# Kernel tuning notes

Hardware: AMD Instinct MI355X
Metric: run time of the kernel (lower is better)

Reference implementation:

```python
import jax, jax.numpy as jnp
import numpy as np

B, P, ENC = 32, 197, 768
EMB, HID, ATT = 512, 512, 256
VOCAB, SLEN = 32000, 41


def setup_inputs() -> dict:
    key = jax.random.key(0)
    ks = jax.random.split(key, 24)
    s = lambda *sh: 1.0 / np.sqrt(sh[0])
    inp = {
        'encoder_out': jax.random.normal(ks[0], (B, P, ENC), dtype=jnp.float32),
        'captions': jax.random.randint(ks[1], (B, SLEN), 0, VOCAB),
        'emb': jax.random.normal(ks[2], (VOCAB, EMB), dtype=jnp.float32) * 0.02,
        # attention
        'W_ea': jax.random.normal(ks[3], (ENC, ATT), dtype=jnp.float32) * s(ENC),
        'b_ea': jnp.zeros((ATT,), jnp.float32),
        'W_da': jax.random.normal(ks[4], (HID, ATT), dtype=jnp.float32) * s(HID),
        'b_da': jnp.zeros((ATT,), jnp.float32),
        'w_fa': jax.random.normal(ks[5], (ATT,), dtype=jnp.float32) * s(ATT),
        'b_fa': jnp.zeros((), jnp.float32),
        # init h/c from mean encoder
        'W_inh': jax.random.normal(ks[6], (ENC, HID), dtype=jnp.float32) * s(ENC),
        'b_inh': jnp.zeros((HID,), jnp.float32),
        'W_inc': jax.random.normal(ks[7], (ENC, HID), dtype=jnp.float32) * s(ENC),
        'b_inc': jnp.zeros((HID,), jnp.float32),
        # gate
        'W_fb': jax.random.normal(ks[8], (HID, ENC), dtype=jnp.float32) * s(HID),
        'b_fb': jnp.zeros((ENC,), jnp.float32),
        # LSTMCell (PyTorch gate order: i, f, g, o)
        'W_ih': jax.random.normal(ks[9], (EMB + ENC, 4 * HID), dtype=jnp.float32) * s(EMB + ENC),
        'b_ih': jnp.zeros((4 * HID,), jnp.float32),
        'W_hh': jax.random.normal(ks[10], (HID, 4 * HID), dtype=jnp.float32) * s(HID),
        'b_hh': jnp.zeros((4 * HID,), jnp.float32),
        # output projection
        'W_out': jax.random.normal(ks[11], (HID, VOCAB), dtype=jnp.float32) * s(HID),
        'b_out': jnp.zeros((VOCAB,), jnp.float32),
    }
    return inp


def reference(encoder_out, captions, emb, W_ea, b_ea, W_da, b_da, w_fa, b_fa,
              W_inh, b_inh, W_inc, b_inc, W_fb, b_fb,
              W_ih, b_ih, W_hh, b_hh, W_out, b_out):
    # dropout is identity (eval mode / p used only in training stochasticity)
    mean_enc = encoder_out.mean(axis=1)                     # (B, ENC)
    h0 = mean_enc @ W_inh + b_inh                           # (B, HID)
    c0 = mean_enc @ W_inc + b_inc
    att1 = encoder_out @ W_ea + b_ea                        # (B, P, ATT) step-invariant
    embs = emb[captions]                                    # (B, S, EMB)
    T = captions.shape[1] - 1
    xs = jnp.swapaxes(embs[:, :T, :], 0, 1)                 # (T, B, EMB)

    def step(carry, x_t):
        h, c = carry
        att2 = h @ W_da + b_da                              # (B, ATT)
        e = jax.nn.relu(att1 + att2[:, None, :]) @ w_fa + b_fa  # (B, P)
        alpha = jax.nn.softmax(e, axis=1)
        awe = jnp.einsum('bp,bpd->bd', alpha, encoder_out)  # (B, ENC)
        gate = jax.nn.sigmoid(h @ W_fb + b_fb)
        awe = gate * awe
        lstm_in = jnp.concatenate([x_t, awe], axis=1)       # (B, EMB+ENC)
        gates = lstm_in @ W_ih + b_ih + h @ W_hh + b_hh     # (B, 4*HID)
        i, f, g, o = jnp.split(gates, 4, axis=1)
        c_new = jax.nn.sigmoid(f) * c + jax.nn.sigmoid(i) * jnp.tanh(g)
        h_new = jax.nn.sigmoid(o) * jnp.tanh(c_new)
        preds = h_new @ W_out + b_out                       # (B, VOCAB)
        return (h_new, c_new), preds

    _, preds = jax.lax.scan(step, (h0, c0), xs)             # (T, B, VOCAB)
    return jnp.swapaxes(preds, 0, 1)                        # (B, T, VOCAB)
```

## Files before the change

kernel.cpp:

```cpp
#include <hip/hip_runtime.h>

#define Bz   32
#define Pz   197
#define ENCz 768
#define EMBz 512
#define HIDz 512
#define ATTz 256
#define VOCz 32000
#define Tz   40

#define NBLK 224

typedef unsigned short ushort_t;
typedef __attribute__((ext_vector_type(8))) short frag_ab;
typedef __attribute__((ext_vector_type(4))) float frag_cd;
typedef __attribute__((ext_vector_type(4))) ushort_t ushort4v;
typedef __attribute__((ext_vector_type(8))) ushort_t ushort8v;

#define MFMA16(a, b, c) __builtin_amdgcn_mfma_f32_16x16x32_bf16((a), (b), (c), 0, 0, 0)

__device__ __forceinline__ float b2f(ushort_t u) {
    return __uint_as_float(((unsigned)u) << 16);
}
__device__ __forceinline__ ushort_t f2bf(float f) {
    unsigned u = __float_as_uint(f);
    unsigned r = (u + 0x7fffu + ((u >> 16) & 1u)) >> 16;
    return (ushort_t)r;
}
__device__ __forceinline__ float sigf(float x) { return 1.f / (1.f + __expf(-x)); }
__device__ __forceinline__ float tanhfast(float x) { return 1.f - 2.f / (__expf(2.f * x) + 1.f); }

__device__ __forceinline__ void st_f32(float* p, float v) {
    __hip_atomic_store(p, v, __ATOMIC_RELAXED, __HIP_MEMORY_SCOPE_AGENT);
}
__device__ __forceinline__ float ld_f32(const float* p) {
    return __hip_atomic_load(p, __ATOMIC_RELAXED, __HIP_MEMORY_SCOPE_AGENT);
}
__device__ __forceinline__ void st_u32(unsigned* p, unsigned v) {
    __hip_atomic_store(p, v, __ATOMIC_RELAXED, __HIP_MEMORY_SCOPE_AGENT);
}
__device__ __forceinline__ unsigned ld_u32(const unsigned* p) {
    return __hip_atomic_load(p, __ATOMIC_RELAXED, __HIP_MEMORY_SCOPE_AGENT);
}
__device__ __forceinline__ frag_ab ldfrag(const ushort_t* p) {
    union { frag_ab f; unsigned long long q[2]; } u;
    u.q[0] = __hip_atomic_load((const unsigned long long*)p, __ATOMIC_RELAXED, __HIP_MEMORY_SCOPE_AGENT);
    u.q[1] = __hip_atomic_load((const unsigned long long*)(p + 4), __ATOMIC_RELAXED, __HIP_MEMORY_SCOPE_AGENT);
    return u.f;
}
__device__ __forceinline__ void arrive(unsigned* slot, unsigned v, int tid) {
    __syncthreads();
    if (tid == 0) {
        asm volatile("s_waitcnt vmcnt(0)" ::: "memory");
        st_u32(slot, v);
    }
}

__global__ void k_binit(unsigned* f) {
    for (int i = threadIdx.x; i < 11264; i += 256) f[i] = 0u;
}

__global__ __launch_bounds__(256) void k_prep(const float* __restrict__ enc, ushort_t* __restrict__ encB,
                                              float* __restrict__ meanE, ushort_t* __restrict__ encTb) {
    __shared__ float tile[32][33];
    const int bid = blockIdx.x, tid = threadIdx.x;
    if (bid < 2364) {
        size_t base = ((size_t)bid * 256 + tid) * 8;
        const float4* src = (const float4*)(enc + base);
        float4 a = src[0], b = src[1];
        ushort8v v;
        v[0] = f2bf(a.x); v[1] = f2bf(a.y); v[2] = f2bf(a.z); v[3] = f2bf(a.w);
        v[4] = f2bf(b.x); v[5] = f2bf(b.y); v[6] = f2bf(b.z); v[7] = f2bf(b.w);
        *(ushort8v*)(encB + base) = v;
    } else if (bid < 2460) {
        int e = (bid - 2364) * 256 + tid;
        int b = e / ENCz, d = e % ENCz;
        const float* p = enc + (size_t)b * Pz * ENCz + d;
        float s = 0.f;
        for (int i = 0; i < Pz; ++i) s += p[i * ENCz];
        meanE[e] = s * (1.f / (float)Pz);
    } else {
        int idx = bid - 2460;
        int d0 = (idx % 24) * 32; int rest = idx / 24;
        int p0 = (rest % 7) * 32; int b = rest / 7;
        int tx = tid & 31, ty = tid >> 5;
#pragma unroll
        for (int i = 0; i < 4; ++i) {
            int p = p0 + ty + i * 8;
            tile[ty + i * 8][tx] = (p < Pz) ? enc[((size_t)b * Pz + p) * ENCz + d0 + tx] : 0.f;
        }
        __syncthreads();
#pragma unroll
        for (int i = 0; i < 4; ++i) {
            int d = d0 + ty + i * 8, p = p0 + tx;
            if (p < 200) encTb[((size_t)b * ENCz + d) * 200 + p] = f2bf(tile[tx][ty + i * 8]);
        }
    }
}

__global__ __launch_bounds__(256) void k_h0c0(const float* __restrict__ meanE,
                                              const float* __restrict__ W_inh, const float* __restrict__ b_inh,
                                              const float* __restrict__ W_inc, const float* __restrict__ b_inc,
                                              float* __restrict__ c_cur, ushort_t* __restrict__ Abuf) {
    __shared__ float msh[ENCz];
    int bid = blockIdx.x, tid = threadIdx.x;
    int b = bid >> 2, seg = bid & 3;
    for (int i = tid; i < ENCz; i += 256) msh[i] = meanE[b * ENCz + i];
    __syncthreads();
    int col = (seg & 1) * 256 + tid;
    bool isc = (seg >> 1) != 0;
    const float* W = isc ? W_inc : W_inh;
    const float* bb = isc ? b_inc : b_inh;
    float a0 = 0.f, a1 = 0.f, a2 = 0.f, a3 = 0.f;
    for (int k = 0; k < ENCz; k += 4) {
        a0 += msh[k + 0] * W[(k + 0) * HIDz + col];
        a1 += msh[k + 1] * W[(k + 1) * HIDz + col];
        a2 += msh[k + 2] * W[(k + 2) * HIDz + col];
        a3 += msh[k + 3] * W[(k + 3) * HIDz + col];
    }
    float acc = a0 + a1 + a2 + a3 + bb[col];
    if (isc) c_cur[b * HIDz + col] = acc;
    else Abuf[b * 1280 + 768 + col] = f2bf(acc);
}

__global__ __launch_bounds__(128) void k_gather(const int* __restrict__ captions, const float* __restrict__ emb,
                                                ushort_t* __restrict__ Xemb) {
    int row = blockIdx.x;
    int t = row >> 5, b = row & 31;
    int cap = captions[b * 41 + t];
    float4 f = *(const float4*)(emb + (size_t)cap * EMBz + threadIdx.x * 4);
    ushort4v v; v[0] = f2bf(f.x); v[1] = f2bf(f.y); v[2] = f2bf(f.z); v[3] = f2bf(f.w);
    *(ushort4v*)(Xemb + (size_t)row * EMBz + threadIdx.x * 4) = v;
}

__global__ __launch_bounds__(256) void k_transpose(const float* __restrict__ in, int R, int C,
                                                   ushort_t* __restrict__ out, int ldo, int koff) {
    __shared__ ushort_t tile[32][33];
    int c0 = blockIdx.x * 32, r0 = blockIdx.y * 32;
    int tx = threadIdx.x & 31, ty = threadIdx.x >> 5;
#pragma unroll
    for (int i = 0; i < 4; ++i) {
        int r = r0 + ty + i * 8;
        tile[ty + i * 8][tx] = f2bf(in[(size_t)r * C + c0 + tx]);
    }
    __syncthreads();
#pragma unroll
    for (int i = 0; i < 4; ++i) {
        int c = c0 + ty + i * 8;
        out[(size_t)c * ldo + koff + r0 + tx] = tile[tx][ty + i * 8];
    }
}

template <int MODE>
__global__ __launch_bounds__(256) void k_gemm(const ushort_t* __restrict__ A, int lda, int M,
                                              const ushort_t* __restrict__ BT, int K,
                                              const float* __restrict__ B1, const float* __restrict__ B2,
                                              void* __restrict__ out, int ldo) {
    __shared__ __align__(16) ushort_t As[128 * 64];
    __shared__ __align__(16) ushort_t Bs[128 * 64];
    const int tid = threadIdx.x;
    const int lane = tid & 63, w = tid >> 6;
    const int wm = w >> 1, wn = w & 1;
    int n0, m0;
    if (MODE == 2) {
        const int total = gridDim.x * gridDim.y;
        const int lin = blockIdx.y * gridDim.x + blockIdx.x;
        const int q = total >> 3, r = total - (q << 3);
        const int xcd = lin & 7, slot = lin >> 3;
        const int L = (xcd < r) ? xcd * (q + 1) + slot : r * (q + 1) + (xcd - r) * q + slot;
        const int nIdx = L / (int)gridDim.y;
        n0 = nIdx * 128; m0 = (L - nIdx * (int)gridDim.y) * 128;
    } else {
        n0 = blockIdx.x * 128; m0 = blockIdx.y * 128;
    }
    const int quad = lane >> 4, c16 = lane & 15;

    frag_cd acc[4][4];
#pragma unroll
    for (int i = 0; i < 4; ++i)
#pragma unroll
        for (int j = 0; j < 4; ++j) acc[i][j] = (frag_cd){0.f, 0.f, 0.f, 0.f};

    for (int k0 = 0; k0 < K; k0 += 64) {
#pragma unroll
        for (int it = 0; it < 4; ++it) {
            int c = tid + it * 256;
            int row = c >> 3, col8 = (c & 7) * 8;
            int gr = m0 + row; gr = gr < M ? gr : M - 1;
            *(frag_ab*)&As[row * 64 + col8] = *(const frag_ab*)&A[(size_t)gr * lda + k0 + col8];
            *(frag_ab*)&Bs[row * 64 + col8] = *(const frag_ab*)&BT[(size_t)(n0 + row) * K + k0 + col8];
        }
        __syncthreads();
#pragma unroll
        for (int kk = 0; kk < 64; kk += 32) {
            int kcol = kk + quad * 8;
            frag_ab af[4], bf[4];
#pragma unroll
            for (int i = 0; i < 4; ++i) af[i] = *(const frag_ab*)&As[(wm * 64 + i * 16 + c16) * 64 + kcol];
#pragma unroll
            for (int j = 0; j < 4; ++j) bf[j] = *(const frag_ab*)&Bs[(wn * 64 + j * 16 + c16) * 64 + kcol];
#pragma unroll
            for (int i = 0; i < 4; ++i)
#pragma unroll
                for (int j = 0; j < 4; ++j) acc[i][j] = MFMA16(af[i], bf[j], acc[i][j]);
        }
        __syncthreads();
    }

#pragma unroll
    for (int i = 0; i < 4; ++i) {
#pragma unroll
        for (int j = 0; j < 4; ++j) {
            int n = n0 + wn * 64 + j * 16 + c16;
            float bias = B1[n];
            if (B2 != nullptr) bias += B2[n];
#pragma unroll
            for (int r = 0; r < 4; ++r) {
                int m = m0 + wm * 64 + i * 16 + quad * 4 + r;
                float v = acc[i][j][r] + bias;
                if (MODE == 0) {
                    if (m < M) ((float*)out)[(size_t)m * ldo + n] = v;
                } else if (MODE == 1) {
                    if (m < M) ((ushort_t*)out)[(size_t)m * ldo + n] = f2bf(v);
                } else {
                    int b = m & 31, t = m >> 5;
                    ((float*)out)[(size_t)b * (Tz * VOCz) + (size_t)t * VOCz + n] = v;
                }
            }
        }
    }
}

__device__ __forceinline__ void gate_calc(const ushort_t* __restrict__ W_preT, const float* __restrict__ b_fb,
                                          const float* hsh, int d0, float* gate_out, int tid) {
    if (tid < 192) {
        const int d = tid >> 1, half = tid & 1;
        const ushort_t* wr = W_preT + (size_t)(256 + d0 + d) * 512 + half * 256;
        const float* hh = hsh + half * 256;
        float a0 = 0.f, a1 = 0.f;
        for (int k = 0; k < 256; k += 8) {
            ushort8v wv8 = *(const ushort8v*)&wr[k];
#pragma unroll
            for (int x = 0; x < 8; ++x) {
                float f = b2f(wv8[x]) * hh[k + x];
                if (x & 1) a1 += f; else a0 += f;
            }
        }
        float s = a0 + a1;
        s += __shfl_xor(s, 1, 64);
        if (half == 0) gate_out[d] = sigf(s + b_fb[d0 + d]);
    }
}

__device__ __forceinline__ void awe_dot(const ushort_t* encS, const float* gate_l, const float* alpha_l,
                                        ushort_t* dst, int tid) {
    if (tid < 192) {
        const int d = tid >> 1, h = tid & 1;
        const int c0 = h ? 13 : 0, c1 = h ? 25 : 13;
        float s = 0.f;
        for (int c = c0; c < c1; ++c) {
            ushort8v v = *(const ushort8v*)&encS[d * 200 + c * 8];
#pragma unroll
            for (int jj = 0; jj < 8; ++jj) s += b2f(v[jj]) * alpha_l[c * 8 + jj];
        }
        s += __shfl_xor(s, 1, 64);
        float gs = s * gate_l[d];
        unsigned pk = f2bf(gs);
        unsigned nb = __shfl_down(pk, 2, 64);
        if ((tid & 3) == 0) st_u32((unsigned*)(dst + d), pk | (nb << 16));
    }
}

__global__ __launch_bounds__(256, 1) void k_recur(
    const ushort_t* __restrict__ att1, const ushort_t* __restrict__ encTb,
    const ushort_t* __restrict__ W_preT, const float* __restrict__ b_da,
    const float* __restrict__ b_fb, const float* __restrict__ w_fa,
    const float* __restrict__ b_fa, const ushort_t* __restrict__ WgT,
    const float* __restrict__ Xih, const float* __restrict__ c0,
    ushort_t* __restrict__ Abuf, float* __restrict__ alpha_buf,
    ushort_t* __restrict__ Hall, unsigned* __restrict__ barflags)
{
    __shared__ __align__(16) char smem[126208];
    float* scratch = (float*)smem;
    char* R = smem + 8192;

    unsigned* flagS = barflags;
    unsigned* flagA = barflags + 4096;
    unsigned* flagE = barflags + 10240;

    const int g = (int)blockIdx.x;
    const int tid = (int)threadIdx.x;
    const int lane = tid & 63, wv = tid >> 6;
    const int quad = lane >> 4, c16 = lane & 15;

    const bool isS3 = (g < 128);
    const bool isE  = (g >= 192);
    const bool dual = (g >= 128 && g < 192);
    const int j0 = g << 2;
    const int task0 = g;
    const int task1 = dual ? 192 + (g - 128) : 0;
    const int b0 = task0 >> 3, d0 = (task0 & 7) * 96;
    const int b1 = task1 >> 3, d1 = (task1 & 7) * 96;
    const int eb = g - 192;

    ushort_t (*Wl)[1288] = (ushort_t(*)[1288])R;
    ushort_t* enc0  = isS3 ? (ushort_t*)(R + 41216) : (ushort_t*)R;
    ushort_t* enc1  = (ushort_t*)(R + 38400);
    ushort_t* att1L = (ushort_t*)R;

    if (isS3) {
        int r = tid >> 4, ch = tid & 15;
        int coln = ((r >> 2) << 9) + j0 + (r & 3);
        const ushort_t* src = WgT + (size_t)coln * 1280 + ch * 80;
        ushort_t* dst = &Wl[r][ch * 80];
#pragma unroll
        for (int i = 0; i < 10; ++i)
            *(ushort8v*)(dst + i * 8) = *(const ushort8v*)(src + i * 8);
    }
    if (!isE) {
        const ushort_t* src = encTb + ((size_t)(b0 * 768 + (task0 & 7) * 96)) * 200;
        for (int i = 0; i < 10; ++i) {
            int c = tid + i * 256;
            if (c < 2400) *(ushort8v*)&enc0[c * 8] = *(const ushort8v*)&src[c * 8];
        }
        if (dual) {
            const ushort_t* src1 = encTb + ((size_t)(b1 * 768 + (task1 & 7) * 96)) * 200;
            for (int i = 0; i < 10; ++i) {
                int c = tid + i * 256;
                if (c < 2400) *(ushort8v*)&enc1[c * 8] = *(const ushort8v*)&src1[c * 8];
            }
        }
    } else {
        for (int i = 0; i < 25; ++i) {
            int c = tid + i * 256;
            if (c < 6304) {
                int p = c >> 5, off = (c & 31) * 8;
                *(ushort8v*)&att1L[p * 264 + off] = *(const ushort8v*)&att1[((size_t)(eb * Pz + p)) * 256 + off];
            }
        }
    }
    float creg = 0.f;
    if (isS3 && tid < 128) creg = c0[(tid >> 2) * HIDz + j0 + (tid & 3)];
    __syncthreads();

    for (int t = 0; t < Tz; ++t) {
        ushort_t* Ab_r = Abuf + (size_t)(t & 1) * 40960;
        ushort_t* Ab_w = Abuf + (size_t)((t + 1) & 1) * 40960;
        const unsigned epoch = (unsigned)(t + 1);

        if (isE) {
            if (t) {
                if (tid < 128) while (ld_u32(&flagS[tid << 5]) < (unsigned)t) __builtin_amdgcn_s_sleep(1);
                __syncthreads();
            }
            if (tid < 64) {
                frag_ab v = ldfrag(Ab_r + eb * 1280 + 768 + tid * 8);
#pragma unroll
                for (int i = 0; i < 8; ++i) scratch[tid * 8 + i] = b2f((ushort_t)v[i]);
            }
            __syncthreads();
            {
                const ushort_t* wr = W_preT + (size_t)tid * 512;
                float a0 = 0.f, a1 = 0.f, a2 = 0.f, a3 = 0.f;
                for (int k = 0; k < 512; k += 16) {
                    ushort8v w0 = *(const ushort8v*)&wr[k];
                    ushort8v w1 = *(const ushort8v*)&wr[k + 8];
#pragma unroll
                    for (int x = 0; x < 8; ++x) {
                        float f0 = b2f(w0[x]) * scratch[k + x];
                        float f1 = b2f(w1[x]) * scratch[k + 8 + x];
                        if (x & 1) { a1 += f0; a3 += f1; } else { a0 += f0; a2 += f1; }
                    }
                }
                scratch[512 + tid] = (a0 + a1) + (a2 + a3) + b_da[tid];
                scratch[768 + tid] = w_fa[tid];
            }
            __syncthreads();
            float ev = -3.0e38f;
            if (tid < Pz) {
                const ushort_t* ar = att1L + tid * 264;
                float s = 0.f;
#pragma unroll
                for (int j8 = 0; j8 < 256; j8 += 8) {
                    ushort8v v = *(const ushort8v*)&ar[j8];
#pragma unroll
                    for (int jj = 0; jj < 8; ++jj)
                        s += fmaxf(b2f(v[jj]) + scratch[512 + j8 + jj], 0.f) * scratch[768 + j8 + jj];
                }
                ev = s + b_fa[0];
            }
            float mv = ev;
            for (int o = 32; o; o >>= 1) mv = fmaxf(mv, __shfl_down(mv, o, 64));
            if (lane == 0) scratch[1024 + wv] = mv;
            __syncthreads();
            const float mx = fmaxf(fmaxf(scratch[1024], scratch[1025]), fmaxf(scratch[1026], scratch[1027]));
            float ex = (tid < Pz) ? __expf(ev - mx) : 0.f;
            float sv = ex;
            for (int o = 32; o; o >>= 1) sv += __shfl_down(sv, o, 64);
            if (lane == 0) scratch[1028 + wv] = sv;
            __syncthreads();
            const float inv = 1.f / (scratch[1028] + scratch[1029] + scratch[1030] + scratch[1031]);
            if (tid < 200) st_f32(&alpha_buf[eb * 200 + tid], ex * inv);
            arrive(&flagE[eb << 5], epoch, tid);
        } else {
            if (t) {
                if (tid < 128) while (ld_u32(&flagS[tid << 5]) < (unsigned)t) __builtin_amdgcn_s_sleep(1);
                __syncthreads();
            }
            if (tid < 64) {
                frag_ab v = ldfrag(Ab_r + b0 * 1280 + 768 + tid * 8);
#pragma unroll
                for (int i = 0; i < 8; ++i) scratch[tid * 8 + i] = b2f((ushort_t)v[i]);
            }
            if (dual && tid >= 64 && tid < 128) {
                int tt = tid - 64;
                frag_ab v = ldfrag(Ab_r + b1 * 1280 + 768 + tt * 8);
#pragma unroll
                for (int i = 0; i < 8; ++i) scratch[512 + tt * 8 + i] = b2f((ushort_t)v[i]);
            }
            __syncthreads();
            gate_calc(W_preT, b_fb, scratch, d0, scratch + 1024, tid);
            if (dual) gate_calc(W_preT, b_fb, scratch + 512, d1, scratch + 1120, tid);
            __syncthreads();
            if (tid == 0)  while (ld_u32(&flagE[b0 << 5]) < epoch) __builtin_amdgcn_s_sleep(1);
            if (dual && tid == 32) while (ld_u32(&flagE[b1 << 5]) < epoch) __builtin_amdgcn_s_sleep(1);
            __syncthreads();
            if (tid < 200) scratch[1280 + tid] = ld_f32(&alpha_buf[b0 * 200 + tid]);
            __syncthreads();
            awe_dot(enc0, scratch + 1024, scratch + 1280, Ab_r + b0 * 1280 + d0, tid);
            if (dual) {
                __syncthreads();
                if (tid < 200) scratch[1280 + tid] = ld_f32(&alpha_buf[b1 * 200 + tid]);
                __syncthreads();
                awe_dot(enc1, scratch + 1120, scratch + 1280, Ab_r + b1 * 1280 + d1, tid);
            }
            arrive(&flagA[g << 5], epoch, tid);
        }

        if (isS3) {
            if (tid < 192) while (ld_u32(&flagA[tid << 5]) < epoch) __builtin_amdgcn_s_sleep(1);
            __syncthreads();
            frag_cd p0 = (frag_cd){0.f, 0.f, 0.f, 0.f};
            frag_cd p1 = (frag_cd){0.f, 0.f, 0.f, 0.f};
            const ushort_t* Ar0 = Ab_r + (size_t)c16 * 1280 + wv * 320 + quad * 8;
            const ushort_t* Ar1 = Ar0 + 16 * 1280;
            const ushort_t* Wr = &Wl[c16][wv * 320 + quad * 8];
#pragma unroll
            for (int ks = 0; ks < 10; ++ks) {
                frag_ab bfr = *(const frag_ab*)(Wr + ks * 32);
                p0 = MFMA16(ldfrag(Ar0 + ks * 32), bfr, p0);
                p1 = MFMA16(ldfrag(Ar1 + ks * 32), bfr, p1);
            }
#pragma unroll
            for (int r = 0; r < 4; ++r) {
                scratch[wv * 512 + (quad * 4 + r) * 16 + c16] = p0[r];
                scratch[wv * 512 + 256 + (quad * 4 + r) * 16 + c16] = p1[r];
            }
            __syncthreads();
            float s0, s1;
            {
                const int mr = tid >> 4, col = tid & 15;
                const int base = mr * 16 + col;
                const int xcol = ((col >> 2) << 9) + j0 + (col & 3);
                s0 = scratch[base] + scratch[512 + base] + scratch[1024 + base] + scratch[1536 + base]
                   + Xih[(size_t)t * 65536 + mr * 2048 + xcol];
                s1 = scratch[256 + base] + scratch[768 + base] + scratch[1280 + base] + scratch[1792 + base]
                   + Xih[(size_t)t * 65536 + (16 + mr) * 2048 + xcol];
            }
            __syncthreads();
            scratch[tid] = s0;
            scratch[256 + tid] = s1;
            __syncthreads();
            if (tid < 128) {
                const int bl = tid >> 2, jj = tid & 3, j = j0 + jj;
                const float iv = scratch[bl * 16 + jj], fv = scratch[bl * 16 + 4 + jj];
                const float gv = scratch[bl * 16 + 8 + jj], ov = scratch[bl * 16 + 12 + jj];
                const float cn = sigf(fv) * creg + sigf(iv) * tanhfast(gv);
                creg = cn;
                const float hn = sigf(ov) * tanhfast(cn);
                const ushort_t hb = f2bf(hn);
                Hall[((size_t)t * 32 + bl) * HIDz + j] = hb;
                unsigned pk = hb;
                unsigned nb = __shfl_down(pk, 1, 64);
                if ((tid & 1) == 0)
                    st_u32((unsigned*)(Ab_w + bl * 1280 + 768 + j), pk | (nb << 16));
            }
            arrive(&flagS[g << 5], epoch, tid);
        }
    }
}

extern "C" void kernel_launch(void* const* d_in, const int* in_sizes, int n_in,
                              void* d_out, int out_size, void* d_ws, size_t ws_size,
                              hipStream_t stream) {
    const float* enc   = (const float*)d_in[0];
    const int*   caps  = (const int*)d_in[1];
    const float* emb   = (const float*)d_in[2];
    const float* W_ea  = (const float*)d_in[3];
    const float* b_ea  = (const float*)d_in[4];
    const float* W_da  = (const float*)d_in[5];
    const float* b_da  = (const float*)d_in[6];
    const float* w_fa  = (const float*)d_in[7];
    const float* b_fa  = (const float*)d_in[8];
    const float* W_inh = (const float*)d_in[9];
    const float* b_inh = (const float*)d_in[10];
    const float* W_inc = (const float*)d_in[11];
    const float* b_inc = (const float*)d_in[12];
    const float* W_fb  = (const float*)d_in[13];
    const float* b_fb  = (const float*)d_in[14];
    const float* W_ih  = (const float*)d_in[15];
    const float* b_ih  = (const float*)d_in[16];
    const float* W_hh  = (const float*)d_in[17];
    const float* b_hh  = (const float*)d_in[18];
    const float* W_out = (const float*)d_in[19];
    const float* b_out = (const float*)d_in[20];

    char* ws = (char*)d_ws;
    ushort_t* att1     = (ushort_t*)(ws + 0);
    ushort_t* Xemb     = (ushort_t*)(ws + 3227648);
    ushort_t* encB     = (ushort_t*)(ws + 4538368);
    float*    Xih      = (float*)(ws + 14221312);
    float*    meanE    = (float*)(ws + 24707072);
    float*    c_cur    = (float*)(ws + 24805376);
    ushort_t* Abuf     = (ushort_t*)(ws + 24870912);
    float*    alpha_buf= (float*)(ws + 25165824);
    ushort_t* Hall     = (ushort_t*)(ws + 25191424);
    ushort_t* WgT      = (ushort_t*)(ws + 26502144);
    ushort_t* W_preT   = (ushort_t*)(ws + 31745024);
    ushort_t* W_eaT    = (ushort_t*)(ws + 32793600);
    ushort_t* W_ihxT   = (ushort_t*)(ws + 33186816);
    ushort_t* W_outT   = (ushort_t*)(ws + 35283968);
    ushort_t* encTb    = (ushort_t*)(ws + 68051968);
    unsigned* barflags = (unsigned*)(ws + 77882368);

    k_binit<<<1, 256, 0, stream>>>(barflags);
    k_prep<<<7836, 256, 0, stream>>>(enc, encB, meanE, encTb);
    k_h0c0<<<128, 256, 0, stream>>>(meanE, W_inh, b_inh, W_inc, b_inc, c_cur, Abuf);
    k_gather<<<1280, 128, 0, stream>>>(caps, emb, Xemb);
    k_transpose<<<dim3(8, 24), 256, 0, stream>>>(W_ea, 768, 256, W_eaT, 768, 0);
    k_transpose<<<dim3(64, 16), 256, 0, stream>>>(W_ih, 512, 2048, W_ihxT, 512, 0);
    k_transpose<<<dim3(64, 24), 256, 0, stream>>>(W_ih + 512 * 2048, 768, 2048, WgT, 1280, 0);
    k_transpose<<<dim3(64, 16), 256, 0, stream>>>(W_hh, 512, 2048, WgT, 1280, 768);
    k_transpose<<<dim3(8, 16), 256, 0, stream>>>(W_da, 512, 256, W_preT, 512, 0);
    k_transpose<<<dim3(24, 16), 256, 0, stream>>>(W_fb, 512, 768, W_preT + 256 * 512, 512, 0);
    k_transpose<<<dim3(1000, 16), 256, 0, stream>>>(W_out, 512, 32000, W_outT, 512, 0);

    k_gemm<1><<<dim3(2, 50), 256, 0, stream>>>(encB, 768, 6304, W_eaT, 768, b_ea, nullptr, att1, 256);
    k_gemm<0><<<dim3(16, 10), 256, 0, stream>>>(Xemb, 512, 1280, W_ihxT, 512, b_ih, b_hh, Xih, 2048);

    hipLaunchKernelGGL(k_recur, dim3(NBLK), dim3(256), 0, stream,
                       att1, encTb, W_preT, b_da, b_fb, w_fa, b_fa, WgT, Xih,
                       c_cur, Abuf, alpha_buf, Hall, barflags);

    k_gemm<2><<<dim3(250, 10), 256, 0, stream>>>(Hall, 512, 1280, W_outT, 512, b_out, nullptr, d_out, VOCz);
}
```

Baseline: 1.462 ms.

## Restructure recurrent kernel into 32 uniform 1024-thread blocks with phased global barriers

The persistent recurrence kernel goes from 224 specialised 256-thread blocks (attention, awe and LSTM roles with separate flag sets) to 32 identical 1024-thread blocks, one per batch row. Each timestep now runs three grid-wide barrier phases. The first is an MFMA pre-projection of h into att2 and the gate. The second does softmax attention plus the gated awe for one batch row, reading encTb directly from global instead of staging it in LDS. The third is an MFMA LSTM gate GEMM over 16 hidden columns per block. The goal is a simpler barrier structure with fewer waiting blocks and more work per block. The cost is three full barriers per step and much lower CU occupancy, since only 32 of the available CUs are used.

```diff
diff --git a/kernel.cpp b/kernel.cpp
--- a/kernel.cpp
+++ b/kernel.cpp
@@ -9,8 +9,6 @@
 #define VOCz 32000
 #define Tz   40
 
-#define NBLK 224
-
 typedef unsigned short ushort_t;
 typedef __attribute__((ext_vector_type(8))) short frag_ab;
 typedef __attribute__((ext_vector_type(4))) float frag_cd;
@@ -57,7 +55,7 @@
 }
 
 __global__ void k_binit(unsigned* f) {
-    for (int i = threadIdx.x; i < 11264; i += 256) f[i] = 0u;
+    for (int i = threadIdx.x; i < 1024; i += 256) f[i] = 0u;
 }
 
 __global__ __launch_bounds__(256) void k_prep(const float* __restrict__ enc, ushort_t* __restrict__ encB,
@@ -101,7 +99,7 @@
 __global__ __launch_bounds__(256) void k_h0c0(const float* __restrict__ meanE,
                                               const float* __restrict__ W_inh, const float* __restrict__ b_inh,
                                               const float* __restrict__ W_inc, const float* __restrict__ b_inc,
-                                              float* __restrict__ c_cur, ushort_t* __restrict__ Abuf) {
+                                              float* __restrict__ c_cur, ushort_t* __restrict__ hbuf) {
     __shared__ float msh[ENCz];
     int bid = blockIdx.x, tid = threadIdx.x;
     int b = bid >> 2, seg = bid & 3;
@@ -120,7 +118,7 @@
     }
     float acc = a0 + a1 + a2 + a3 + bb[col];
     if (isc) c_cur[b * HIDz + col] = acc;
-    else Abuf[b * 1280 + 768 + col] = f2bf(acc);
+    else hbuf[b * HIDz + col] = f2bf(acc);
 }
 
 __global__ __launch_bounds__(128) void k_gather(const int* __restrict__ captions, const float* __restrict__ emb,
@@ -231,262 +229,159 @@
     }
 }
 
-__device__ __forceinline__ void gate_calc(const ushort_t* __restrict__ W_preT, const float* __restrict__ b_fb,
-                                          const float* hsh, int d0, float* gate_out, int tid) {
-    if (tid < 192) {
-        const int d = tid >> 1, half = tid & 1;
-        const ushort_t* wr = W_preT + (size_t)(256 + d0 + d) * 512 + half * 256;
-        const float* hh = hsh + half * 256;
-        float a0 = 0.f, a1 = 0.f;
-        for (int k = 0; k < 256; k += 8) {
-            ushort8v wv8 = *(const ushort8v*)&wr[k];
-#pragma unroll
-            for (int x = 0; x < 8; ++x) {
-                float f = b2f(wv8[x]) * hh[k + x];
-                if (x & 1) a1 += f; else a0 += f;
-            }
-        }
-        float s = a0 + a1;
-        s += __shfl_xor(s, 1, 64);
-        if (half == 0) gate_out[d] = sigf(s + b_fb[d0 + d]);
-    }
-}
-
-__device__ __forceinline__ void awe_dot(const ushort_t* encS, const float* gate_l, const float* alpha_l,
-                                        ushort_t* dst, int tid) {
-    if (tid < 192) {
-        const int d = tid >> 1, h = tid & 1;
-        const int c0 = h ? 13 : 0, c1 = h ? 25 : 13;
-        float s = 0.f;
-        for (int c = c0; c < c1; ++c) {
-            ushort8v v = *(const ushort8v*)&encS[d * 200 + c * 8];
-#pragma unroll
-            for (int jj = 0; jj < 8; ++jj) s += b2f(v[jj]) * alpha_l[c * 8 + jj];
-        }
-        s += __shfl_xor(s, 1, 64);
-        float gs = s * gate_l[d];
-        unsigned pk = f2bf(gs);
-        unsigned nb = __shfl_down(pk, 2, 64);
-        if ((tid & 3) == 0) st_u32((unsigned*)(dst + d), pk | (nb << 16));
-    }
-}
-
-__global__ __launch_bounds__(256, 1) void k_recur(
+__global__ __launch_bounds__(1024, 1) void k_recur(
     const ushort_t* __restrict__ att1, const ushort_t* __restrict__ encTb,
     const ushort_t* __restrict__ W_preT, const float* __restrict__ b_da,
     const float* __restrict__ b_fb, const float* __restrict__ w_fa,
     const float* __restrict__ b_fa, const ushort_t* __restrict__ WgT,
     const float* __restrict__ Xih, const float* __restrict__ c0,
-    ushort_t* __restrict__ Abuf, float* __restrict__ alpha_buf,
-    ushort_t* __restrict__ Hall, unsigned* __restrict__ barflags)
+    float* __restrict__ pre_buf, ushort_t* __restrict__ gawe_buf,
+    ushort_t* __restrict__ hbuf, ushort_t* __restrict__ Hall,
+    unsigned* __restrict__ flags)
 {
-    __shared__ __align__(16) char smem[126208];
-    float* scratch = (float*)smem;
-    char* R = smem + 8192;
-
-    unsigned* flagS = barflags;
-    unsigned* flagA = barflags + 4096;
-    unsigned* flagE = barflags + 10240;
+    __shared__ __align__(16) ushort_t att1L[197 * 264];
+    __shared__ float wfa_sh[256];
+    __shared__ float att2_sh[256];
+    __shared__ float gate_sh[768];
+    __shared__ float alpha_sh[200];
+    __shared__ float g4[2][4][32][16];
+    __shared__ float red[16];
 
     const int g = (int)blockIdx.x;
     const int tid = (int)threadIdx.x;
     const int lane = tid & 63, wv = tid >> 6;
     const int quad = lane >> 4, c16 = lane & 15;
 
-    const bool isS3 = (g < 128);
-    const bool isE  = (g >= 192);
-    const bool dual = (g >= 128 && g < 192);
-    const int j0 = g << 2;
-    const int task0 = g;
-    const int task1 = dual ? 192 + (g - 128) : 0;
-    const int b0 = task0 >> 3, d0 = (task0 & 7) * 96;
-    const int b1 = task1 >> 3, d1 = (task1 & 7) * 96;
-    const int eb = g - 192;
-
-    ushort_t (*Wl)[1288] = (ushort_t(*)[1288])R;
-    ushort_t* enc0  = isS3 ? (ushort_t*)(R + 41216) : (ushort_t*)R;
-    ushort_t* enc1  = (ushort_t*)(R + 38400);
-    ushort_t* att1L = (ushort_t*)R;
-
-    if (isS3) {
-        int r = tid >> 4, ch = tid & 15;
-        int coln = ((r >> 2) << 9) + j0 + (r & 3);
-        const ushort_t* src = WgT + (size_t)coln * 1280 + ch * 80;
-        ushort_t* dst = &Wl[r][ch * 80];
-#pragma unroll
-        for (int i = 0; i < 10; ++i)
-            *(ushort8v*)(dst + i * 8) = *(const ushort8v*)(src + i * 8);
-    }
-    if (!isE) {
-        const ushort_t* src = encTb + ((size_t)(b0 * 768 + (task0 & 7) * 96)) * 200;
-        for (int i = 0; i < 10; ++i) {
-            int c = tid + i * 256;
-            if (c < 2400) *(ushort8v*)&enc0[c * 8] = *(const ushort8v*)&src[c * 8];
-        }
-        if (dual) {
-            const ushort_t* src1 = encTb + ((size_t)(b1 * 768 + (task1 & 7) * 96)) * 200;
-            for (int i = 0; i < 10; ++i) {
-                int c = tid + i * 256;
-                if (c < 2400) *(ushort8v*)&enc1[c * 8] = *(const ushort8v*)&src1[c * 8];
-            }
-        }
-    } else {
-        for (int i = 0; i < 25; ++i) {
-            int c = tid + i * 256;
-            if (c < 6304) {
-                int p = c >> 5, off = (c & 31) * 8;
-                *(ushort8v*)&att1L[p * 264 + off] = *(const ushort8v*)&att1[((size_t)(eb * Pz + p)) * 256 + off];
-            }
-        }
-    }
+    for (int i = 0; i < 7; ++i) {
+        int c = tid + i * 1024;
+        if (c < 6304) {
+            int p = c >> 5, off = (c & 31) * 8;
+            *(ushort8v*)&att1L[p * 264 + off] =
+                *(const ushort8v*)&att1[((size_t)(g * Pz + p)) * 256 + off];
+        }
+    }
+    if (tid < 256) wfa_sh[tid] = w_fa[tid];
     float creg = 0.f;
-    if (isS3 && tid < 128) creg = c0[(tid >> 2) * HIDz + j0 + (tid & 3)];
+    if (tid < 512) creg = c0[(tid >> 4) * HIDz + g * 16 + (tid & 15)];
+    const float bfa = b_fa[0];
     __syncthreads();
 
     for (int t = 0; t < Tz; ++t) {
-        ushort_t* Ab_r = Abuf + (size_t)(t & 1) * 40960;
-        ushort_t* Ab_w = Abuf + (size_t)((t + 1) & 1) * 40960;
-        const unsigned epoch = (unsigned)(t + 1);
-
-        if (isE) {
-            if (t) {
-                if (tid < 128) while (ld_u32(&flagS[tid << 5]) < (unsigned)t) __builtin_amdgcn_s_sleep(1);
-                __syncthreads();
-            }
-            if (tid < 64) {
-                frag_ab v = ldfrag(Ab_r + eb * 1280 + 768 + tid * 8);
-#pragma unroll
-                for (int i = 0; i < 8; ++i) scratch[tid * 8 + i] = b2f((ushort_t)v[i]);
-            }
+        if (t) {
+            if (tid < 32) while (ld_u32(&flags[tid << 5]) < (unsigned)(3 * t)) __builtin_amdgcn_s_sleep(2);
             __syncthreads();
-            {
-                const ushort_t* wr = W_preT + (size_t)tid * 512;
-                float a0 = 0.f, a1 = 0.f, a2 = 0.f, a3 = 0.f;
-                for (int k = 0; k < 512; k += 16) {
-                    ushort8v w0 = *(const ushort8v*)&wr[k];
-                    ushort8v w1 = *(const ushort8v*)&wr[k + 8];
-#pragma unroll
-                    for (int x = 0; x < 8; ++x) {
-                        float f0 = b2f(w0[x]) * scratch[k + x];
-                        float f1 = b2f(w1[x]) * scratch[k + 8 + x];
-                        if (x & 1) { a1 += f0; a3 += f1; } else { a0 += f0; a2 += f1; }
-                    }
-                }
-                scratch[512 + tid] = (a0 + a1) + (a2 + a3) + b_da[tid];
-                scratch[768 + tid] = w_fa[tid];
-            }
-            __syncthreads();
-            float ev = -3.0e38f;
-            if (tid < Pz) {
-                const ushort_t* ar = att1L + tid * 264;
-                float s = 0.f;
-#pragma unroll
-                for (int j8 = 0; j8 < 256; j8 += 8) {
-                    ushort8v v = *(const ushort8v*)&ar[j8];
-#pragma unroll
-                    for (int jj = 0; jj < 8; ++jj)
-                        s += fmaxf(b2f(v[jj]) + scratch[512 + j8 + jj], 0.f) * scratch[768 + j8 + jj];
-                }
-                ev = s + b_fa[0];
-            }
-            float mv = ev;
-            for (int o = 32; o; o >>= 1) mv = fmaxf(mv, __shfl_down(mv, o, 64));
-            if (lane == 0) scratch[1024 + wv] = mv;
-            __syncthreads();
-            const float mx = fmaxf(fmaxf(scratch[1024], scratch[1025]), fmaxf(scratch[1026], scratch[1027]));
-            float ex = (tid < Pz) ? __expf(ev - mx) : 0.f;
-            float sv = ex;
-            for (int o = 32; o; o >>= 1) sv += __shfl_down(sv, o, 64);
-            if (lane == 0) scratch[1028 + wv] = sv;
-            __syncthreads();
-            const float inv = 1.f / (scratch[1028] + scratch[1029] + scratch[1030] + scratch[1031]);
-            if (tid < 200) st_f32(&alpha_buf[eb * 200 + tid], ex * inv);
-            arrive(&flagE[eb << 5], epoch, tid);
-        } else {
-            if (t) {
-                if (tid < 128) while (ld_u32(&flagS[tid << 5]) < (unsigned)t) __builtin_amdgcn_s_sleep(1);
-                __syncthreads();
-            }
-            if (tid < 64) {
-                frag_ab v = ldfrag(Ab_r + b0 * 1280 + 768 + tid * 8);
-#pragma unroll
-                for (int i = 0; i < 8; ++i) scratch[tid * 8 + i] = b2f((ushort_t)v[i]);
-            }
-            if (dual && tid >= 64 && tid < 128) {
-                int tt = tid - 64;
-                frag_ab v = ldfrag(Ab_r + b1 * 1280 + 768 + tt * 8);
-#pragma unroll
-                for (int i = 0; i < 8; ++i) scratch[512 + tt * 8 + i] = b2f((ushort_t)v[i]);
-            }
-            __syncthreads();
-            gate_calc(W_preT, b_fb, scratch, d0, scratch + 1024, tid);
-            if (dual) gate_calc(W_preT, b_fb, scratch + 512, d1, scratch + 1120, tid);
-            __syncthreads();
-            if (tid == 0)  while (ld_u32(&flagE[b0 << 5]) < epoch) __builtin_amdgcn_s_sleep(1);
-            if (dual && tid == 32) while (ld_u32(&flagE[b1 << 5]) < epoch) __builtin_amdgcn_s_sleep(1);
-            __syncthreads();
-            if (tid < 200) scratch[1280 + tid] = ld_f32(&alpha_buf[b0 * 200 + tid]);
-            __syncthreads();
-            awe_dot(enc0, scratch + 1024, scratch + 1280, Ab_r + b0 * 1280 + d0, tid);
-            if (dual) {
-                __syncthreads();
-                if (tid < 200) scratch[1280 + tid] = ld_f32(&alpha_buf[b1 * 200 + tid]);
-                __syncthreads();
-                awe_dot(enc1, scratch + 1120, scratch + 1280, Ab_r + b1 * 1280 + d1, tid);
-            }
-            arrive(&flagA[g << 5], epoch, tid);
-        }
-
-        if (isS3) {
-            if (tid < 192) while (ld_u32(&flagA[tid << 5]) < epoch) __builtin_amdgcn_s_sleep(1);
-            __syncthreads();
-            frag_cd p0 = (frag_cd){0.f, 0.f, 0.f, 0.f};
-            frag_cd p1 = (frag_cd){0.f, 0.f, 0.f, 0.f};
-            const ushort_t* Ar0 = Ab_r + (size_t)c16 * 1280 + wv * 320 + quad * 8;
-            const ushort_t* Ar1 = Ar0 + 16 * 1280;
-            const ushort_t* Wr = &Wl[c16][wv * 320 + quad * 8];
-#pragma unroll
-            for (int ks = 0; ks < 10; ++ks) {
-                frag_ab bfr = *(const frag_ab*)(Wr + ks * 32);
-                p0 = MFMA16(ldfrag(Ar0 + ks * 32), bfr, p0);
-                p1 = MFMA16(ldfrag(Ar1 + ks * 32), bfr, p1);
-            }
+        }
+        if (wv < 4) {
+            const int mt = wv >> 1, nt = wv & 1;
+            frag_cd acc = (frag_cd){0.f, 0.f, 0.f, 0.f};
+            const ushort_t* hrow = hbuf + (size_t)(mt * 16 + c16) * HIDz;
+            const ushort_t* wrow = W_preT + (size_t)(g * 32 + nt * 16 + c16) * HIDz;
+#pragma unroll
+            for (int kk = 0; kk < 512; kk += 32) {
+                frag_ab af = ldfrag(hrow + kk + quad * 8);
+                frag_ab bf = *(const frag_ab*)&wrow[kk + quad * 8];
+                acc = MFMA16(af, bf, acc);
+            }
+            const int n = g * 32 + nt * 16 + c16;
+            const float bias = (n < 256) ? b_da[n] : b_fb[n - 256];
 #pragma unroll
             for (int r = 0; r < 4; ++r) {
-                scratch[wv * 512 + (quad * 4 + r) * 16 + c16] = p0[r];
-                scratch[wv * 512 + 256 + (quad * 4 + r) * 16 + c16] = p1[r];
-            }
-            __syncthreads();
-            float s0, s1;
-            {
-                const int mr = tid >> 4, col = tid & 15;
-                const int base = mr * 16 + col;
-                const int xcol = ((col >> 2) << 9) + j0 + (col & 3);
-                s0 = scratch[base] + scratch[512 + base] + scratch[1024 + base] + scratch[1536 + base]
-                   + Xih[(size_t)t * 65536 + mr * 2048 + xcol];
-                s1 = scratch[256 + base] + scratch[768 + base] + scratch[1280 + base] + scratch[1792 + base]
-                   + Xih[(size_t)t * 65536 + (16 + mr) * 2048 + xcol];
-            }
-            __syncthreads();
-            scratch[tid] = s0;
-            scratch[256 + tid] = s1;
-            __syncthreads();
-            if (tid < 128) {
-                const int bl = tid >> 2, jj = tid & 3, j = j0 + jj;
-                const float iv = scratch[bl * 16 + jj], fv = scratch[bl * 16 + 4 + jj];
-                const float gv = scratch[bl * 16 + 8 + jj], ov = scratch[bl * 16 + 12 + jj];
-                const float cn = sigf(fv) * creg + sigf(iv) * tanhfast(gv);
-                creg = cn;
-                const float hn = sigf(ov) * tanhfast(cn);
-                const ushort_t hb = f2bf(hn);
-                Hall[((size_t)t * 32 + bl) * HIDz + j] = hb;
-                unsigned pk = hb;
-                unsigned nb = __shfl_down(pk, 1, 64);
-                if ((tid & 1) == 0)
-                    st_u32((unsigned*)(Ab_w + bl * 1280 + 768 + j), pk | (nb << 16));
-            }
-            arrive(&flagS[g << 5], epoch, tid);
-        }
+                int m = mt * 16 + quad * 4 + r;
+                float v = acc[r] + bias;
+                if (n >= 256) v = sigf(v);
+                st_f32(&pre_buf[m * 1024 + n], v);
+            }
+        }
+        arrive(&flags[g << 5], (unsigned)(3 * t + 1), tid);
+
+        if (tid < 32) while (ld_u32(&flags[tid << 5]) < (unsigned)(3 * t + 1)) __builtin_amdgcn_s_sleep(2);
+        __syncthreads();
+        if (tid < 256) att2_sh[tid] = ld_f32(&pre_buf[g * 1024 + tid]);
+        else gate_sh[tid - 256] = ld_f32(&pre_buf[g * 1024 + tid]);
+        __syncthreads();
+        float ev = -3.0e38f;
+        if (tid < Pz) {
+            const ushort_t* ar = att1L + tid * 264;
+            float s = 0.f;
+#pragma unroll
+            for (int j8 = 0; j8 < 256; j8 += 8) {
+                ushort8v v = *(const ushort8v*)&ar[j8];
+#pragma unroll
+                for (int jj = 0; jj < 8; ++jj)
+                    s += fmaxf(b2f(v[jj]) + att2_sh[j8 + jj], 0.f) * wfa_sh[j8 + jj];
+            }
+            ev = s + bfa;
+        }
+        float mv = ev;
+        for (int o = 32; o; o >>= 1) mv = fmaxf(mv, __shfl_down(mv, o, 64));
+        if (lane == 0 && wv < 4) red[wv] = mv;
+        __syncthreads();
+        const float mx = fmaxf(fmaxf(red[0], red[1]), fmaxf(red[2], red[3]));
+        float ex = (tid < Pz) ? __expf(ev - mx) : 0.f;
+        float sv = ex;
+        for (int o = 32; o; o >>= 1) sv += __shfl_down(sv, o, 64);
+        if (lane == 0 && wv < 4) red[4 + wv] = sv;
+        __syncthreads();
+        const float inv = 1.f / (red[4] + red[5] + red[6] + red[7]);
+        if (tid < 200) alpha_sh[tid] = (tid < Pz) ? ex * inv : 0.f;
+        __syncthreads();
+        if (tid < 768) {
+            const ushort_t* er = encTb + ((size_t)(g * ENCz + tid)) * 200;
+            float s = 0.f;
+#pragma unroll
+            for (int c = 0; c < 25; ++c) {
+                ushort8v v = *(const ushort8v*)&er[c * 8];
+#pragma unroll
+                for (int jj = 0; jj < 8; ++jj) s += b2f(v[jj]) * alpha_sh[c * 8 + jj];
+            }
+            float gs = s * gate_sh[tid];
+            unsigned pk = f2bf(gs);
+            unsigned nb = __shfl_down(pk, 1, 64);
+            if ((tid & 1) == 0) st_u32((unsigned*)&gawe_buf[g * 768 + tid], pk | (nb << 16));
+        }
+        arrive(&flags[g << 5], (unsigned)(3 * t + 2), tid);
+
+        if (tid < 32) while (ld_u32(&flags[tid << 5]) < (unsigned)(3 * t + 2)) __builtin_amdgcn_s_sleep(2);
+        __syncthreads();
+        {
+            const int kh = wv & 1, q = (wv >> 1) & 3, mt = wv >> 3;
+            frag_cd acc = (frag_cd){0.f, 0.f, 0.f, 0.f};
+            const int jcol = q * 512 + g * 16 + c16;
+            const ushort_t* wrow = WgT + (size_t)jcol * 1280;
+            const int arow = mt * 16 + c16;
+            const ushort_t* grow = gawe_buf + (size_t)arow * 768;
+            const ushort_t* hrow = hbuf + (size_t)arow * 512;
+#pragma unroll
+            for (int ki = 0; ki < 20; ++ki) {
+                const int k = kh * 640 + ki * 32;
+                frag_ab af = (k < 768) ? ldfrag(grow + k + quad * 8)
+                                       : ldfrag(hrow + (k - 768) + quad * 8);
+                frag_ab bf = *(const frag_ab*)&wrow[k + quad * 8];
+                acc = MFMA16(af, bf, acc);
+            }
+#pragma unroll
+            for (int r = 0; r < 4; ++r)
+                g4[kh][q][mt * 16 + quad * 4 + r][c16] = acc[r];
+        }
+        __syncthreads();
+        if (tid < 512) {
+            const int m = tid >> 4, jj = tid & 15;
+            const float* xr = Xih + (size_t)t * 65536 + m * 2048 + g * 16 + jj;
+            const float iv = g4[0][0][m][jj] + g4[1][0][m][jj] + xr[0];
+            const float fv = g4[0][1][m][jj] + g4[1][1][m][jj] + xr[512];
+            const float gv = g4[0][2][m][jj] + g4[1][2][m][jj] + xr[1024];
+            const float ov = g4[0][3][m][jj] + g4[1][3][m][jj] + xr[1536];
+            const float cn = sigf(fv) * creg + sigf(iv) * tanhfast(gv);
+            creg = cn;
+            const float hn = sigf(ov) * tanhfast(cn);
+            const ushort_t hb = f2bf(hn);
+            Hall[((size_t)t * 32 + m) * HIDz + g * 16 + jj] = hb;
+            unsigned pk = hb;
+            unsigned nb = __shfl_down(pk, 1, 64);
+            if ((tid & 1) == 0)
+                st_u32((unsigned*)&hbuf[m * 512 + g * 16 + jj], pk | (nb << 16));
+        }
+        arrive(&flags[g << 5], (unsigned)(3 * t + 3), tid);
     }
 }
 
@@ -522,8 +417,10 @@
     float*    Xih      = (float*)(ws + 14221312);
     float*    meanE    = (float*)(ws + 24707072);
     float*    c_cur    = (float*)(ws + 24805376);
-    ushort_t* Abuf     = (ushort_t*)(ws + 24870912);
-    float*    alpha_buf= (float*)(ws + 25165824);
+    float*    pre_buf  = (float*)(ws + 24870912);
+    ushort_t* gawe_buf = (ushort_t*)(ws + 25001984);
+    ushort_t* hbuf     = (ushort_t*)(ws + 25051136);
+    unsigned* flags    = (unsigned*)(ws + 25083904);
     ushort_t* Hall     = (ushort_t*)(ws + 25191424);
     ushort_t* WgT      = (ushort_t*)(ws + 26502144);
     ushort_t* W_preT   = (ushort_t*)(ws + 31745024);
@@ -531,11 +428,10 @@
     ushort_t* W_ihxT   = (ushort_t*)(ws + 33186816);
     ushort_t* W_outT   = (ushort_t*)(ws + 35283968);
     ushort_t* encTb    = (ushort_t*)(ws + 68051968);
-    unsigned* barflags = (unsigned*)(ws + 77882368);
-
-    k_binit<<<1, 256, 0, stream>>>(barflags);
+
+    k_binit<<<1, 256, 0, stream>>>(flags);
     k_prep<<<7836, 256, 0, stream>>>(enc, encB, meanE, encTb);
-    k_h0c0<<<128, 256, 0, stream>>>(meanE, W_inh, b_inh, W_inc, b_inc, c_cur, Abuf);
+    k_h0c0<<<128, 256, 0, stream>>>(meanE, W_inh, b_inh, W_inc, b_inc, c_cur, hbuf);
     k_gather<<<1280, 128, 0, stream>>>(caps, emb, Xemb);
     k_transpose<<<dim3(8, 24), 256, 0, stream>>>(W_ea, 768, 256, W_eaT, 768, 0);
     k_transpose<<<dim3(64, 16), 256, 0, stream>>>(W_ih, 512, 2048, W_ihxT, 512, 0);
@@ -548,9 +444,9 @@
     k_gemm<1><<<dim3(2, 50), 256, 0, stream>>>(encB, 768, 6304, W_eaT, 768, b_ea, nullptr, att1, 256);
     k_gemm<0><<<dim3(16, 10), 256, 0, stream>>>(Xemb, 512, 1280, W_ihxT, 512, b_ih, b_hh, Xih, 2048);
 
-    hipLaunchKernelGGL(k_recur, dim3(NBLK), dim3(256), 0, stream,
+    hipLaunchKernelGGL(k_recur, dim3(32), dim3(1024), 0, stream,
                        att1, encTb, W_preT, b_da, b_fb, w_fa, b_fa, WgT, Xih,
-                       c_cur, Abuf, alpha_buf, Hall, barflags);
+                       c_cur, pre_buf, gawe_buf, hbuf, Hall, flags);
 
     k_gemm<2><<<dim3(250, 10), 256, 0, stream>>>(Hall, 512, 1280, W_outT, 512, b_out, nullptr, d_out, VOCz);
 }
```

Result: slower. 2.504 ms (+71.3%).
